# Kernel optimization log

Measured on AMD Instinct MI355X. Metric: run time of the kernel, lower is better.

Reference implementation:

```python
import jax, jax.numpy as jnp
import numpy as np
from jax import lax

NB, D_MODEL, D_INNER, D_STATE, K, L, BATCH, NCLS, DT_RANK = 3, 512, 1024, 8, 4, 2048, 4, 10, 32


def setup_inputs() -> dict:
    key = jax.random.key(0)
    ks = jax.random.split(key, 12)
    s = 0.02
    inp = {
        "x": jax.random.normal(ks[0], (BATCH, L, D_MODEL), jnp.float32),
        "in_proj_w": s * jax.random.normal(ks[1], (NB, D_MODEL, 2 * D_INNER), jnp.float32),
        "conv_w": s * jax.random.normal(ks[2], (NB, D_INNER, K), jnp.float32),
        "conv_b": jnp.zeros((NB, D_INNER), jnp.float32),
        "x_proj_w": s * jax.random.normal(ks[3], (NB, D_INNER, DT_RANK + 2 * D_STATE), jnp.float32),
        "dt_proj_w": s * jax.random.normal(ks[4], (NB, DT_RANK, D_INNER), jnp.float32),
        "dt_proj_b": jnp.full((NB, D_INNER), -4.0, jnp.float32),
        "A_log": jnp.broadcast_to(jnp.log(jnp.arange(1, D_STATE + 1, dtype=jnp.float32)), (NB, D_INNER, D_STATE)).copy(),
        "D": jnp.ones((NB, D_INNER), jnp.float32),
        "out_proj_w": s * jax.random.normal(ks[5], (NB, D_INNER, D_MODEL), jnp.float32),
        "cls_w": s * jax.random.normal(ks[6], (D_MODEL, NCLS), jnp.float32),
        "cls_b": jnp.zeros((NCLS,), jnp.float32),
    }
    return inp


def _mamba_block(x, Wi, cw, cb, Wx, Wdt, bdt, A_log, Dp, Wo):
    # x: [B, L, d_model]
    Bsz, Lx, _ = x.shape
    d_inner = Dp.shape[0]
    d_state = A_log.shape[-1]
    dt_rank = Wdt.shape[0]
    xz = x @ Wi                               # [B, L, 2*d_inner]
    u, z = jnp.split(xz, 2, axis=-1)
    # causal depthwise conv1d over time
    uc = jnp.swapaxes(u, 1, 2)                # [B, d_inner, L]
    k = cw.shape[-1]
    uc = lax.conv_general_dilated(uc, cw[:, None, :], window_strides=(1,),
                                  padding=[(k - 1, 0)], feature_group_count=d_inner,
                                  dimension_numbers=("NCH", "OIH", "NCH"))
    u = jax.nn.silu(jnp.swapaxes(uc, 1, 2) + cb)   # [B, L, d_inner]
    dbl = u @ Wx                                   # [B, L, dt_rank + 2*d_state]
    dt = dbl[..., :dt_rank]
    Bm = dbl[..., dt_rank:dt_rank + d_state]
    Cm = dbl[..., dt_rank + d_state:]
    delta = jax.nn.softplus(dt @ Wdt + bdt)        # [B, L, d_inner]
    A = -jnp.exp(A_log)                            # [d_inner, d_state]

    def step(h, inp):
        d_t, B_t, C_t, u_t = inp                   # [B,d],[B,n],[B,n],[B,d]
        h = jnp.exp(d_t[..., None] * A) * h + (d_t * u_t)[..., None] * B_t[:, None, :]
        return h, jnp.einsum("bdn,bn->bd", h, C_t)

    xs = (jnp.swapaxes(delta, 0, 1), jnp.swapaxes(Bm, 0, 1),
          jnp.swapaxes(Cm, 0, 1), jnp.swapaxes(u, 0, 1))
    h0 = jnp.zeros((Bsz, d_inner, d_state), x.dtype)
    _, ys = lax.scan(step, h0, xs)                 # ys: [L, B, d_inner]
    y = jnp.swapaxes(ys, 0, 1) + u * Dp
    y = y * jax.nn.silu(z)
    return x + y @ Wo                              # residual


def reference(x, in_proj_w, conv_w, conv_b, x_proj_w, dt_proj_w, dt_proj_b, A_log, D, out_proj_w, cls_w, cls_b):
    nb = in_proj_w.shape[0]
    for i in range(nb):
        x = _mamba_block(x, in_proj_w[i], conv_w[i], conv_b[i], x_proj_w[i],
                         dt_proj_w[i], dt_proj_b[i], A_log[i], D[i], out_proj_w[i])
    pooled = jnp.mean(x, axis=1)                   # AdaptiveAvgPool1d(1) over seq
    return pooled @ cls_w + cls_b                  # [B, num_classes]
```

## Files before the change

kernel.cpp:

```cpp
#include <hip/hip_runtime.h>
#include <cstddef>
#include <cstdint>

#define L_SEQ   2048
#define BATCH_N 4
#define DMODEL  512
#define DINNER  1024
#define DSTATE  8
#define KCONV   4
#define DTRANK  32
#define NBLK    3
#define NCLS_N  10
#define MROWS   (BATCH_N * L_SEQ)
#define DBLW    48
#define NSPLIT  8

#define LC2 16
#define NC2 (L_SEQ / LC2)
#define VD  2
#define SCAN_THREADS 512
#define SCAN_WAVES   (SCAN_THREADS / 64)

typedef __attribute__((ext_vector_type(8))) short bf16x8;
typedef __attribute__((ext_vector_type(4))) short bf16x4;
typedef __attribute__((ext_vector_type(2))) short bf16x2;
typedef __attribute__((ext_vector_type(4))) float f32x4;

__device__ __forceinline__ float sigmoid_fast(float x) { return 1.f / (1.f + __expf(-x)); }
__device__ __forceinline__ float silu_fast(float x)    { return x * sigmoid_fast(x); }
__device__ __forceinline__ float softplus_fast(float x){
    return fmaxf(x, 0.f) + __logf(1.f + __expf(-fabsf(x)));
}
__device__ __forceinline__ float exp2_fast(float x) {
#if __has_builtin(__builtin_amdgcn_exp2f)
    return __builtin_amdgcn_exp2f(x);
#else
    return __expf(x * 0.69314718055994531f);
#endif
}
#define LOG2E 1.44269504088896341f

__device__ __forceinline__ unsigned short f2bf(float f) {
    union { float f; uint32_t u; } v; v.f = f;
    const uint32_t u = v.u;
    return (unsigned short)((u + 0x7fffu + ((u >> 16) & 1u)) >> 16);
}
__device__ __forceinline__ float bf2f(unsigned short h) {
    union { uint32_t u; float f; } v; v.u = ((uint32_t)h) << 16;
    return v.f;
}
__device__ __forceinline__ float bf2f_s(short h) { return bf2f((unsigned short)h); }

__device__ __forceinline__ void load_lds16(const void* g, void* l) {
    __builtin_amdgcn_global_load_lds(
        (const __attribute__((address_space(1))) unsigned int*)g,
        (__attribute__((address_space(3))) unsigned int*)l,
        16, 0, 0);
}

template <int K, int NT, int EPI>
__global__ __launch_bounds__(256) void gemm_bf16(
    const unsigned short* __restrict__ A, int lda,
    const unsigned short* __restrict__ Bt, int ldb,
    int ldc,
    unsigned short* __restrict__ Obf,
    float* __restrict__ pool)
{
    constexpr int BCH   = NT / 8;
    constexpr int NTW   = NT / 32;
    constexpr int STAGE = 8192 + NT * 64;
    constexpr int EPIL  = 128 * (NT + 8);
    constexpr int SMEM  = (STAGE > EPIL) ? STAGE : EPIL;
    __shared__ unsigned short sMem[SMEM];
    unsigned short* sA = sMem;
    unsigned short* sB = sMem + 8192;

    const int tid  = threadIdx.x;
    const int lane = tid & 63;
    const int wave = tid >> 6;
    const int m0 = blockIdx.y * 128;
    const int n0 = blockIdx.x * NT;
    const int wm = (wave >> 1) * 64;
    const int wn = (wave & 1) * (NT / 2);
    const int lm = lane & 15;
    const int lq = lane >> 4;

    const int srow = lane >> 3;
    const int scol = ((lane & 7) ^ srow) * 8;

    f32x4 acc[4][NTW];
    #pragma unroll
    for (int i = 0; i < 4; ++i)
        #pragma unroll
        for (int j = 0; j < NTW; ++j) acc[i][j] = (f32x4){0.f, 0.f, 0.f, 0.f};

    for (int k0 = 0; k0 < K; k0 += 64) {
        #pragma unroll
        for (int c = wave; c < 16; c += 4)
            load_lds16(A + (size_t)(m0 + c * 8 + srow) * lda + k0 + scol, &sA[c * 512]);
        #pragma unroll
        for (int c = wave; c < BCH; c += 4)
            load_lds16(Bt + (size_t)(n0 + c * 8 + srow) * ldb + k0 + scol, &sB[c * 512]);
        __syncthreads();
        #pragma unroll
        for (int ks = 0; ks < 2; ++ks) {
            bf16x8 aF[4], bF[NTW];
            #pragma unroll
            for (int mt = 0; mt < 4; ++mt) {
                const int row = wm + mt * 16 + lm;
                aF[mt] = *(const bf16x8*)&sA[row * 64 + (((ks * 4 + lq) ^ (lm & 7)) * 8)];
            }
            #pragma unroll
            for (int nt = 0; nt < NTW; ++nt) {
                const int row = wn + nt * 16 + lm;
                bF[nt] = *(const bf16x8*)&sB[row * 64 + (((ks * 4 + lq) ^ (lm & 7)) * 8)];
            }
            #pragma unroll
            for (int mt = 0; mt < 4; ++mt)
                #pragma unroll
                for (int nt = 0; nt < NTW; ++nt)
                    acc[mt][nt] = __builtin_amdgcn_mfma_f32_16x16x32_bf16(
                        aF[mt], bF[nt], acc[mt][nt], 0, 0, 0);
        }
        __syncthreads();
    }

    unsigned short* sOut = sMem;
    #pragma unroll
    for (int mt = 0; mt < 4; ++mt) {
        #pragma unroll
        for (int nt = 0; nt < NTW; ++nt) {
            #pragma unroll
            for (int r = 0; r < 4; ++r) {
                const int row = wm + mt * 16 + lq * 4 + r;
                const int col = wn + nt * 16 + lm;
                float v = acc[mt][nt][r];
                if (EPI >= 2) {
                    const size_t gi = (size_t)(m0 + row) * ldc + n0 + col;
                    v += bf2f(Obf[gi]);
                }
                sOut[row * (NT + 8) + col] = f2bf(v);
            }
        }
    }
    __syncthreads();
    #pragma unroll
    for (int j = 0; j < NT / 16; ++j) {
        const int idx = j * 256 + tid;
        const int row = idx / (NT / 8);
        const int cpos = (idx % (NT / 8)) * 8;
        *(bf16x8*)&Obf[(size_t)(m0 + row) * ldc + n0 + cpos] =
            *(const bf16x8*)&sOut[row * (NT + 8) + cpos];
    }
    if (EPI == 3) {
        const int b = m0 >> 11;
        const int col = tid & (NT - 1);
        const int q = tid / NT;
        constexpr int RPQ = 128 / (256 / NT);
        float s = 0.f;
        #pragma unroll
        for (int r = q * RPQ; r < (q + 1) * RPQ; ++r)
            s += bf2f(sOut[r * (NT + 8) + col]);
        atomicAdd(&pool[b * DMODEL + n0 + col], s);
    }
}

__global__ __launch_bounds__(256) void gemm_xproj(
    const unsigned short* __restrict__ ub,
    const unsigned short* __restrict__ Wxt,
    float* __restrict__ dblsum)
{
    const int tid = threadIdx.x, lane = tid & 63, wave = tid >> 6;
    const int lm = lane & 15, lq = lane >> 4;
    const int rowA = blockIdx.x * 128 + wave * 32;
    const int split = blockIdx.y;
    const int k0 = split * (DINNER / NSPLIT);

    f32x4 acc[2][3];
    #pragma unroll
    for (int i = 0; i < 2; ++i)
        #pragma unroll
        for (int j = 0; j < 3; ++j) acc[i][j] = (f32x4){0.f, 0.f, 0.f, 0.f};

    #pragma unroll
    for (int kk = 0; kk < DINNER / NSPLIT; kk += 32) {
        const int k = k0 + kk;
        bf16x8 aF[2], bF[3];
        #pragma unroll
        for (int mt = 0; mt < 2; ++mt)
            aF[mt] = *(const bf16x8*)&ub[(size_t)(rowA + mt * 16 + lm) * DINNER + k + lq * 8];
        #pragma unroll
        for (int nt = 0; nt < 3; ++nt)
            bF[nt] = *(const bf16x8*)&Wxt[(size_t)(nt * 16 + lm) * DINNER + k + lq * 8];
        #pragma unroll
        for (int mt = 0; mt < 2; ++mt)
            #pragma unroll
            for (int nt = 0; nt < 3; ++nt)
                acc[mt][nt] = __builtin_amdgcn_mfma_f32_16x16x32_bf16(
                    aF[mt], bF[nt], acc[mt][nt], 0, 0, 0);
    }
    #pragma unroll
    for (int mt = 0; mt < 2; ++mt)
        #pragma unroll
        for (int nt = 0; nt < 3; ++nt)
            #pragma unroll
            for (int r = 0; r < 4; ++r)
                atomicAdd(&dblsum[(size_t)(rowA + mt * 16 + lq * 4 + r) * DBLW
                                  + nt * 16 + lm], acc[mt][nt][r]);
}

__global__ __launch_bounds__(256) void transpose_cast(
    const float* __restrict__ in, unsigned short* __restrict__ out,
    int Kdim, int Ndim, size_t in_stride, size_t out_stride)
{
    __shared__ float s[32][33];
    const float* ip = in + blockIdx.z * in_stride;
    unsigned short* op = out + blockIdx.z * out_stride;
    const int bx = blockIdx.x * 32;
    const int by = blockIdx.y * 32;
    const int t = threadIdx.x;
    const int r = t >> 3;
    const int c4 = (t & 7) * 4;

    const int row = by + r;
    if (bx + c4 + 3 < Ndim) {
        float4 v = *(const float4*)&ip[(size_t)row * Ndim + bx + c4];
        s[r][c4 + 0] = v.x; s[r][c4 + 1] = v.y; s[r][c4 + 2] = v.z; s[r][c4 + 3] = v.w;
    } else {
        for (int i = 0; i < 4; ++i) {
            const int col = bx + c4 + i;
            s[r][c4 + i] = (col < Ndim) ? ip[(size_t)row * Ndim + col] : 0.f;
        }
    }
    __syncthreads();
    if (bx + r < Ndim) {
        unsigned short w0 = f2bf(s[c4 + 0][r]), w1 = f2bf(s[c4 + 1][r]);
        unsigned short w2 = f2bf(s[c4 + 2][r]), w3 = f2bf(s[c4 + 3][r]);
        uint2 pk;
        pk.x = (uint32_t)w0 | ((uint32_t)w1 << 16);
        pk.y = (uint32_t)w2 | ((uint32_t)w3 << 16);
        *(uint2*)&op[(size_t)(bx + r) * Kdim + by + c4] = pk;
    }
}

__global__ void cast_init(const float* __restrict__ in, unsigned short* __restrict__ outb,
                          float* __restrict__ pooled_accum, int n4) {
    const int i = blockIdx.x * 256 + threadIdx.x;
    if (i < BATCH_N * DMODEL / 4)
        ((f32x4*)pooled_accum)[i] = (f32x4){0.f, 0.f, 0.f, 0.f};
    if (i >= n4) return;
    float4 v = ((const float4*)in)[i];
    uint2 pk;
    pk.x = (uint32_t)f2bf(v.x) | ((uint32_t)f2bf(v.y) << 16);
    pk.y = (uint32_t)f2bf(v.z) | ((uint32_t)f2bf(v.w) << 16);
    ((uint2*)outb)[i] = pk;
}

__global__ void conv_w_transpose(const float* __restrict__ cw, float* __restrict__ cwt) {
    const int i = blockIdx.x * 256 + threadIdx.x;
    if (i >= NBLK * DINNER * KCONV) return;
    const int blk = i >> 12;
    const int rem = i & 4095;
    const int d = rem >> 2;
    const int k = rem & 3;
    cwt[blk * 4096 + k * DINNER + d] = cw[blk * 4096 + d * KCONV + k];
}

__global__ __launch_bounds__(256) void conv_silu_kernel(
    const unsigned short* __restrict__ xz,
    const float* __restrict__ cwt,
    const float* __restrict__ cb,
    unsigned short* __restrict__ ub,
    float* __restrict__ dblsum)
{
    const int idx = blockIdx.x * 256 + threadIdx.x;
    if (idx < MROWS * DBLW / 4)
        ((f32x4*)dblsum)[idx] = (f32x4){0.f, 0.f, 0.f, 0.f};

    const int dv = idx & 127;
    const int m  = idx >> 7;
    const int t  = m & (L_SEQ - 1);
    const int d0 = dv * 8;

    float acc[8];
    {
        float4 c0 = *(const float4*)&cb[d0];
        float4 c1 = *(const float4*)&cb[d0 + 4];
        acc[0] = c0.x; acc[1] = c0.y; acc[2] = c0.z; acc[3] = c0.w;
        acc[4] = c1.x; acc[5] = c1.y; acc[6] = c1.z; acc[7] = c1.w;
    }
    #pragma unroll
    for (int k = 0; k < KCONV; ++k) {
        const int tt = t + k - (KCONV - 1);
        if (tt >= 0) {
            bf16x8 xv = *(const bf16x8*)&xz[(size_t)(m - t + tt) * (2 * DINNER) + d0];
            float4 w0 = *(const float4*)&cwt[k * DINNER + d0];
            float4 w1 = *(const float4*)&cwt[k * DINNER + d0 + 4];
            acc[0] = fmaf(bf2f_s(xv[0]), w0.x, acc[0]);
            acc[1] = fmaf(bf2f_s(xv[1]), w0.y, acc[1]);
            acc[2] = fmaf(bf2f_s(xv[2]), w0.z, acc[2]);
            acc[3] = fmaf(bf2f_s(xv[3]), w0.w, acc[3]);
            acc[4] = fmaf(bf2f_s(xv[4]), w1.x, acc[4]);
            acc[5] = fmaf(bf2f_s(xv[5]), w1.y, acc[5]);
            acc[6] = fmaf(bf2f_s(xv[6]), w1.z, acc[6]);
            acc[7] = fmaf(bf2f_s(xv[7]), w1.w, acc[7]);
        }
    }
    bf16x8 o;
    #pragma unroll
    for (int j = 0; j < 8; ++j) o[j] = (short)f2bf(silu_fast(acc[j]));
    *(bf16x8*)&ub[(size_t)m * DINNER + d0] = o;
}

__device__ __forceinline__ void dt_recompute_lds(
    unsigned short* sDelta,
    const float* __restrict__ dblsum,
    const unsigned short* __restrict__ Wdtt,
    const float* __restrict__ bdt,
    size_t m0, int lane, int wave)
{
    const int lm = lane & 15, lq = lane >> 4;
    bf16x8 aF;
    {
        const float* p = &dblsum[(m0 + lm) * DBLW + lq * 8];
        float4 x0 = *(const float4*)p;
        float4 x1 = *(const float4*)(p + 4);
        aF[0] = (short)f2bf(x0.x); aF[1] = (short)f2bf(x0.y);
        aF[2] = (short)f2bf(x0.z); aF[3] = (short)f2bf(x0.w);
        aF[4] = (short)f2bf(x1.x); aF[5] = (short)f2bf(x1.y);
        aF[6] = (short)f2bf(x1.z); aF[7] = (short)f2bf(x1.w);
    }
    constexpr int NPW = DINNER / (16 * SCAN_WAVES);
    #pragma unroll
    for (int nt = 0; nt < NPW; ++nt) {
        const int col16 = wave * (DINNER / SCAN_WAVES) + nt * 16;
        bf16x8 bF = *(const bf16x8*)&Wdtt[(size_t)(col16 + lm) * DTRANK + lq * 8];
        f32x4 acc = (f32x4){0.f, 0.f, 0.f, 0.f};
        acc = __builtin_amdgcn_mfma_f32_16x16x32_bf16(aF, bF, acc, 0, 0, 0);
        const float bias = bdt[col16 + lm];
        #pragma unroll
        for (int r = 0; r < 4; ++r)
            sDelta[(lq * 4 + r) * DINNER + col16 + lm] =
                f2bf(softplus_fast(acc[r] + bias));
    }
}

__global__ __launch_bounds__(SCAN_THREADS) void scan_chunk_kernel(
    const unsigned short* __restrict__ ub,
    const float* __restrict__ dblsum,
    const unsigned short* __restrict__ Wdtt,
    const float* __restrict__ bdt,
    const float* __restrict__ A_log,
    float* __restrict__ PSbuf)
{
    const int c = blockIdx.x;
    const int b = blockIdx.y;
    const int tid = threadIdx.x;
    const int lane = tid & 63;
    const int wave = tid >> 6;
    const int d0 = tid * VD;

    __shared__ unsigned short sDelta[LC2 * DINNER];
    __shared__ float sB[LC2][DSTATE];

    const size_t m0 = (size_t)b * L_SEQ + c * LC2;

    dt_recompute_lds(sDelta, dblsum, Wdtt, bdt, m0, lane, wave);
    if (tid < LC2 * DSTATE) {
        const int r = tid >> 3, n = tid & 7;
        sB[r][n] = dblsum[(m0 + r) * DBLW + DTRANK + n];
    }
    __syncthreads();

    float a[DSTATE * VD], P[DSTATE * VD], S[DSTATE * VD];
    #pragma unroll
    for (int n = 0; n < DSTATE; ++n)
        #pragma unroll
        for (int v = 0; v < VD; ++v) {
            a[n * VD + v] = -__expf(A_log[(d0 + v) * DSTATE + n]) * LOG2E;
            P[n * VD + v] = 1.f;
            S[n * VD + v] = 0.f;
        }

    for (int r = 0; r < LC2; ++r) {
        const size_t m = m0 + r;
        bf16x2 dv = *(const bf16x2*)&sDelta[r * DINNER + d0];
        bf16x2 uv = *(const bf16x2*)&ub[m * DINNER + d0];
        float dt[VD], du[VD];
        #pragma unroll
        for (int v = 0; v < VD; ++v) {
            dt[v] = bf2f_s(dv[v]);
            du[v] = dt[v] * bf2f_s(uv[v]);
        }
        #pragma unroll
        for (int n = 0; n < DSTATE; ++n) {
            const float bn = sB[r][n];
            #pragma unroll
            for (int v = 0; v < VD; ++v) {
                const float e = exp2_fast(dt[v] * a[n * VD + v]);
                S[n * VD + v] = fmaf(e, S[n * VD + v], du[v] * bn);
                P[n * VD + v] *= e;
            }
        }
    }

    const size_t nb = (size_t)(b * NC2 + c) * DSTATE;
    #pragma unroll
    for (int n = 0; n < DSTATE; ++n) {
        float* dst = &PSbuf[(nb + n) * (DINNER * 2) + (size_t)d0 * 2];
        *(f32x4*)dst =
            (f32x4){P[n * VD + 0], S[n * VD + 0], P[n * VD + 1], S[n * VD + 1]};
    }
}

__global__ __launch_bounds__(64) void scan_combine_kernel(
    const float* __restrict__ PSbuf,
    float* __restrict__ Hbuf)
{
    const int d = blockIdx.x * 64 + threadIdx.x;
    const int n = blockIdx.y;
    const int b = blockIdx.z;

    float h = 0.f;
    #pragma unroll 8
    for (int c = 0; c < NC2; ++c) {
        const size_t row = (size_t)(b * NC2 + c) * DSTATE + n;
        const float2 ps = *(const float2*)&PSbuf[row * (DINNER * 2) + (size_t)d * 2];
        Hbuf[row * DINNER + d] = h;
        h = fmaf(ps.x, h, ps.y);
    }
}

__global__ __launch_bounds__(SCAN_THREADS) void scan_out_kernel(
    const unsigned short* __restrict__ ub,
    const float* __restrict__ dblsum,
    const unsigned short* __restrict__ Wdtt,
    const float* __restrict__ bdt,
    const unsigned short* __restrict__ xz,
    const float* __restrict__ A_log,
    const float* __restrict__ Dp,
    const float* __restrict__ Hin,
    unsigned short* __restrict__ ybuf)
{
    const int c = blockIdx.x;
    const int b = blockIdx.y;
    const int tid = threadIdx.x;
    const int lane = tid & 63;
    const int wave = tid >> 6;
    const int d0 = tid * VD;

    __shared__ unsigned short sDelta[LC2 * DINNER];
    __shared__ float sB[LC2][DSTATE];
    __shared__ float sC[LC2][DSTATE];

    const size_t m0 = (size_t)b * L_SEQ + c * LC2;

    dt_recompute_lds(sDelta, dblsum, Wdtt, bdt, m0, lane, wave);
    if (tid < LC2 * 2 * DSTATE) {
        const int r = tid >> 4, j = tid & 15;
        const float v = dblsum[(m0 + r) * DBLW + DTRANK + j];
        if (j < DSTATE) sB[r][j] = v;
        else            sC[r][j - DSTATE] = v;
    }
    __syncthreads();

    float a[DSTATE * VD], h[DSTATE * VD];
    const size_t base = ((size_t)(b * NC2 + c) * DSTATE) * DINNER + d0;
    #pragma unroll
    for (int n = 0; n < DSTATE; ++n) {
        float2 hv = *(const float2*)&Hin[base + (size_t)n * DINNER];
        h[n * VD + 0] = hv.x; h[n * VD + 1] = hv.y;
        #pragma unroll
        for (int v = 0; v < VD; ++v)
            a[n * VD + v] = -__expf(A_log[(d0 + v) * DSTATE + n]) * LOG2E;
    }
    float Dd[VD];
    {
        float2 dv2 = *(const float2*)&Dp[d0];
        Dd[0] = dv2.x; Dd[1] = dv2.y;
    }

    for (int r = 0; r < LC2; ++r) {
        const size_t m = m0 + r;
        bf16x2 dv = *(const bf16x2*)&sDelta[r * DINNER + d0];
        bf16x2 uv = *(const bf16x2*)&ub[m * DINNER + d0];
        bf16x2 zv = *(const bf16x2*)&xz[m * (2 * DINNER) + DINNER + d0];
        float dt[VD], ut[VD], du[VD], acc[VD];
        #pragma unroll
        for (int v = 0; v < VD; ++v) {
            dt[v] = bf2f_s(dv[v]);
            ut[v] = bf2f_s(uv[v]);
            du[v] = dt[v] * ut[v];
            acc[v] = 0.f;
        }
        #pragma unroll
        for (int n = 0; n < DSTATE; ++n) {
            const float bn = sB[r][n];
            const float cn = sC[r][n];
            #pragma unroll
            for (int v = 0; v < VD; ++v) {
                const float e = exp2_fast(dt[v] * a[n * VD + v]);
                h[n * VD + v] = fmaf(e, h[n * VD + v], du[v] * bn);
                acc[v] = fmaf(h[n * VD + v], cn, acc[v]);
            }
        }
        bf16x2 o;
        #pragma unroll
        for (int v = 0; v < VD; ++v)
            o[v] = (short)f2bf(fmaf(ut[v], Dd[v], acc[v]) * silu_fast(bf2f_s(zv[v])));
        *(bf16x2*)&ybuf[m * DINNER + d0] = o;
    }
}

__global__ __launch_bounds__(512) void pool_cls_kernel(
    const float* __restrict__ pooled_accum,
    const float* __restrict__ w,
    const float* __restrict__ bias,
    float* __restrict__ out)
{
    __shared__ float sp[DMODEL];
    const int b = blockIdx.x;
    const int dm = threadIdx.x;
    sp[dm] = pooled_accum[b * DMODEL + dm] * (1.f / (float)L_SEQ);
    __syncthreads();
    if (dm < NCLS_N) {
        float acc = bias[dm];
        for (int k = 0; k < DMODEL; ++k)
            acc = fmaf(sp[k], w[k * NCLS_N + dm], acc);
        out[b * NCLS_N + dm] = acc;
    }
}

extern "C" void kernel_launch(void* const* d_in, const int* in_sizes, int n_in,
                              void* d_out, int out_size, void* d_ws, size_t ws_size,
                              hipStream_t stream) {
    const float* x_in      = (const float*)d_in[0];
    const float* in_proj_w = (const float*)d_in[1];
    const float* conv_w    = (const float*)d_in[2];
    const float* conv_b    = (const float*)d_in[3];
    const float* x_proj_w  = (const float*)d_in[4];
    const float* dt_proj_w = (const float*)d_in[5];
    const float* dt_proj_b = (const float*)d_in[6];
    const float* A_log     = (const float*)d_in[7];
    const float* Dp        = (const float*)d_in[8];
    const float* out_proj_w= (const float*)d_in[9];
    const float* cls_w     = (const float*)d_in[10];
    const float* cls_b     = (const float*)d_in[11];
    float* out = (float*)d_out;

    char* w = (char*)d_ws;
    auto alloc = [&](size_t bytes) { char* p = w; w += (bytes + 255) & ~(size_t)255; return p; };
    unsigned short* xz_bf  = (unsigned short*)alloc((size_t)MROWS * 2 * DINNER * 2);
    unsigned short* ub     = (unsigned short*)alloc((size_t)MROWS * DINNER * 2);
    float*          dblsum = (float*)         alloc((size_t)MROWS * DBLW * 4);
    float*          PSbuf  = (float*)         alloc((size_t)BATCH_N * NC2 * DSTATE * DINNER * 2 * 4);
    float*          Hbuf   = (float*)         alloc((size_t)BATCH_N * NC2 * DSTATE * DINNER * 4);
    unsigned short* xb     = (unsigned short*)alloc((size_t)MROWS * DMODEL * 2);
    unsigned short* ybuf   = (unsigned short*)alloc((size_t)MROWS * DINNER * 2);
    unsigned short* Wit    = (unsigned short*)alloc((size_t)NBLK * 2048 * 512 * 2);
    unsigned short* Wot    = (unsigned short*)alloc((size_t)NBLK * 512 * 1024 * 2);
    unsigned short* Wxt    = (unsigned short*)alloc((size_t)NBLK * DBLW * 1024 * 2);
    unsigned short* Wdtt   = (unsigned short*)alloc((size_t)NBLK * 1024 * DTRANK * 2);
    float*          cwt    = (float*)         alloc((size_t)NBLK * KCONV * DINNER * 4);
    float*          pooled = (float*)         alloc((size_t)BATCH_N * DMODEL * 4);

    cast_init<<<(MROWS * DMODEL / 4) / 256, 256, 0, stream>>>(
        x_in, xb, pooled, MROWS * DMODEL / 4);
    transpose_cast<<<dim3(2048 / 32, 512 / 32, NBLK), 256, 0, stream>>>(
        in_proj_w, Wit, 512, 2048, (size_t)512 * 2048, (size_t)2048 * 512);
    transpose_cast<<<dim3(512 / 32, 1024 / 32, NBLK), 256, 0, stream>>>(
        out_proj_w, Wot, 1024, 512, (size_t)1024 * 512, (size_t)512 * 1024);
    transpose_cast<<<dim3(2, 1024 / 32, NBLK), 256, 0, stream>>>(
        x_proj_w, Wxt, 1024, DBLW, (size_t)1024 * DBLW, (size_t)DBLW * 1024);
    transpose_cast<<<dim3(1024 / 32, 1, NBLK), 256, 0, stream>>>(
        dt_proj_w, Wdtt, DTRANK, 1024, (size_t)DTRANK * 1024, (size_t)1024 * DTRANK);
    conv_w_transpose<<<(NBLK * DINNER * KCONV + 255) / 256, 256, 0, stream>>>(conv_w, cwt);

    for (int blk = 0; blk < NBLK; ++blk) {
        const unsigned short* Wit_b  = Wit  + (size_t)blk * 2048 * 512;
        const unsigned short* Wot_b  = Wot  + (size_t)blk * 512 * 1024;
        const unsigned short* Wxt_b  = Wxt  + (size_t)blk * DBLW * 1024;
        const unsigned short* Wdtt_b = Wdtt + (size_t)blk * 1024 * DTRANK;
        const float* cwt_b = cwt + (size_t)blk * KCONV * DINNER;
        const float* cb  = conv_b    + (size_t)blk * DINNER;
        const float* bdt = dt_proj_b + (size_t)blk * DINNER;
        const float* Al  = A_log     + (size_t)blk * DINNER * DSTATE;
        const float* Dv  = Dp        + (size_t)blk * DINNER;

        gemm_bf16<512, 128, 0><<<dim3(2048 / 128, MROWS / 128), 256, 0, stream>>>(
            xb, DMODEL, Wit_b, DMODEL, 2 * DINNER, xz_bf, nullptr);
        conv_silu_kernel<<<(MROWS * 128) / 256, 256, 0, stream>>>(
            xz_bf, cwt_b, cb, ub, dblsum);
        gemm_xproj<<<dim3(MROWS / 128, NSPLIT), 256, 0, stream>>>(ub, Wxt_b, dblsum);
        {
            dim3 gridA(NC2, BATCH_N);
            scan_chunk_kernel<<<gridA, SCAN_THREADS, 0, stream>>>(
                ub, dblsum, Wdtt_b, bdt, Al, PSbuf);
            scan_combine_kernel<<<dim3(DINNER / 64, DSTATE, BATCH_N), 64, 0, stream>>>(
                PSbuf, Hbuf);
            scan_out_kernel<<<gridA, SCAN_THREADS, 0, stream>>>(
                ub, dblsum, Wdtt_b, bdt, xz_bf, Al, Dv, Hbuf, ybuf);
        }
        if (blk < NBLK - 1)
            gemm_bf16<1024, 64, 2><<<dim3(DMODEL / 64, MROWS / 128), 256, 0, stream>>>(
                ybuf, DINNER, Wot_b, DINNER, DMODEL, xb, nullptr);
        else
            gemm_bf16<1024, 64, 3><<<dim3(DMODEL / 64, MROWS / 128), 256, 0, stream>>>(
                ybuf, DINNER, Wot_b, DINNER, DMODEL, xb, pooled);
    }

    pool_cls_kernel<<<BATCH_N, DMODEL, 0, stream>>>(pooled, cls_w, cls_b, out);
}
```

Measured before the change: 533.4 us.

## Replace split-K atomics with partial buffers and parallelize chunk-prefix combine

The x_proj split-K GEMM now writes each split's partial sums to its own buffer instead of atomically adding into a zeroed buffer, and the scan kernels sum the eight partials when they load. The conv kernel no longer zeroes that buffer. The chunk decay product is computed as exp2 of a times the summed dt instead of a running per-step product. The cross-chunk combine kernel splits the 128 chunks into 8 groups per block, building group prefixes in LDS so the serial chain is shorter. The cost is more reads of the partial buffers in the scan kernels and extra workspace.

```diff
diff --git a/kernel.cpp b/kernel.cpp
--- a/kernel.cpp
+++ b/kernel.cpp
@@ -21,6 +21,9 @@
 #define SCAN_THREADS 512
 #define SCAN_WAVES   (SCAN_THREADS / 64)
 
+#define CGRP 8
+#define CPG  (NC2 / CGRP)
+
 typedef __attribute__((ext_vector_type(8))) short bf16x8;
 typedef __attribute__((ext_vector_type(4))) short bf16x4;
 typedef __attribute__((ext_vector_type(2))) short bf16x2;
@@ -168,7 +171,7 @@
 __global__ __launch_bounds__(256) void gemm_xproj(
     const unsigned short* __restrict__ ub,
     const unsigned short* __restrict__ Wxt,
-    float* __restrict__ dblsum)
+    float* __restrict__ Xp)
 {
     const int tid = threadIdx.x, lane = tid & 63, wave = tid >> 6;
     const int lm = lane & 15, lq = lane >> 4;
@@ -199,14 +202,15 @@
                 acc[mt][nt] = __builtin_amdgcn_mfma_f32_16x16x32_bf16(
                     aF[mt], bF[nt], acc[mt][nt], 0, 0, 0);
     }
+    float* dst = Xp + (size_t)split * MROWS * DBLW;
     #pragma unroll
     for (int mt = 0; mt < 2; ++mt)
         #pragma unroll
         for (int nt = 0; nt < 3; ++nt)
             #pragma unroll
             for (int r = 0; r < 4; ++r)
-                atomicAdd(&dblsum[(size_t)(rowA + mt * 16 + lq * 4 + r) * DBLW
-                                  + nt * 16 + lm], acc[mt][nt][r]);
+                dst[(size_t)(rowA + mt * 16 + lq * 4 + r) * DBLW
+                    + nt * 16 + lm] = acc[mt][nt][r];
 }
 
 __global__ __launch_bounds__(256) void transpose_cast(
@@ -270,13 +274,9 @@
     const unsigned short* __restrict__ xz,
     const float* __restrict__ cwt,
     const float* __restrict__ cb,
-    unsigned short* __restrict__ ub,
-    float* __restrict__ dblsum)
+    unsigned short* __restrict__ ub)
 {
     const int idx = blockIdx.x * 256 + threadIdx.x;
-    if (idx < MROWS * DBLW / 4)
-        ((f32x4*)dblsum)[idx] = (f32x4){0.f, 0.f, 0.f, 0.f};
-
     const int dv = idx & 127;
     const int m  = idx >> 7;
     const int t  = m & (L_SEQ - 1);
@@ -314,22 +314,25 @@
 
 __device__ __forceinline__ void dt_recompute_lds(
     unsigned short* sDelta,
-    const float* __restrict__ dblsum,
+    const float* __restrict__ Xp,
     const unsigned short* __restrict__ Wdtt,
     const float* __restrict__ bdt,
     size_t m0, int lane, int wave)
 {
     const int lm = lane & 15, lq = lane >> 4;
-    bf16x8 aF;
-    {
-        const float* p = &dblsum[(m0 + lm) * DBLW + lq * 8];
+    float x[8] = {0.f, 0.f, 0.f, 0.f, 0.f, 0.f, 0.f, 0.f};
+    #pragma unroll
+    for (int sp = 0; sp < NSPLIT; ++sp) {
+        const float* p = &Xp[((size_t)sp * MROWS + m0 + lm) * DBLW + lq * 8];
         float4 x0 = *(const float4*)p;
         float4 x1 = *(const float4*)(p + 4);
-        aF[0] = (short)f2bf(x0.x); aF[1] = (short)f2bf(x0.y);
-        aF[2] = (short)f2bf(x0.z); aF[3] = (short)f2bf(x0.w);
-        aF[4] = (short)f2bf(x1.x); aF[5] = (short)f2bf(x1.y);
-        aF[6] = (short)f2bf(x1.z); aF[7] = (short)f2bf(x1.w);
-    }
+        x[0] += x0.x; x[1] += x0.y; x[2] += x0.z; x[3] += x0.w;
+        x[4] += x1.x; x[5] += x1.y; x[6] += x1.z; x[7] += x1.w;
+    }
+    bf16x8 aF;
+    #pragma unroll
+    for (int j = 0; j < 8; ++j) aF[j] = (short)f2bf(x[j]);
+
     constexpr int NPW = DINNER / (16 * SCAN_WAVES);
     #pragma unroll
     for (int nt = 0; nt < NPW; ++nt) {
@@ -347,7 +350,7 @@
 
 __global__ __launch_bounds__(SCAN_THREADS) void scan_chunk_kernel(
     const unsigned short* __restrict__ ub,
-    const float* __restrict__ dblsum,
+    const float* __restrict__ Xp,
     const unsigned short* __restrict__ Wdtt,
     const float* __restrict__ bdt,
     const float* __restrict__ A_log,
@@ -365,20 +368,26 @@
 
     const size_t m0 = (size_t)b * L_SEQ + c * LC2;
 
-    dt_recompute_lds(sDelta, dblsum, Wdtt, bdt, m0, lane, wave);
+    dt_recompute_lds(sDelta, Xp, Wdtt, bdt, m0, lane, wave);
     if (tid < LC2 * DSTATE) {
         const int r = tid >> 3, n = tid & 7;
-        sB[r][n] = dblsum[(m0 + r) * DBLW + DTRANK + n];
+        float s = 0.f;
+        #pragma unroll
+        for (int sp = 0; sp < NSPLIT; ++sp)
+            s += Xp[((size_t)sp * MROWS + m0 + r) * DBLW + DTRANK + n];
+        sB[r][n] = s;
     }
     __syncthreads();
 
-    float a[DSTATE * VD], P[DSTATE * VD], S[DSTATE * VD];
+    float a[DSTATE * VD], S[DSTATE * VD];
+    float dtsum[VD];
+    #pragma unroll
+    for (int v = 0; v < VD; ++v) dtsum[v] = 0.f;
     #pragma unroll
     for (int n = 0; n < DSTATE; ++n)
         #pragma unroll
         for (int v = 0; v < VD; ++v) {
             a[n * VD + v] = -__expf(A_log[(d0 + v) * DSTATE + n]) * LOG2E;
-            P[n * VD + v] = 1.f;
             S[n * VD + v] = 0.f;
         }
 
@@ -391,6 +400,7 @@
         for (int v = 0; v < VD; ++v) {
             dt[v] = bf2f_s(dv[v]);
             du[v] = dt[v] * bf2f_s(uv[v]);
+            dtsum[v] += dt[v];
         }
         #pragma unroll
         for (int n = 0; n < DSTATE; ++n) {
@@ -399,7 +409,6 @@
             for (int v = 0; v < VD; ++v) {
                 const float e = exp2_fast(dt[v] * a[n * VD + v]);
                 S[n * VD + v] = fmaf(e, S[n * VD + v], du[v] * bn);
-                P[n * VD + v] *= e;
             }
         }
     }
@@ -407,24 +416,46 @@
     const size_t nb = (size_t)(b * NC2 + c) * DSTATE;
     #pragma unroll
     for (int n = 0; n < DSTATE; ++n) {
+        const float P0 = exp2_fast(a[n * VD + 0] * dtsum[0]);
+        const float P1 = exp2_fast(a[n * VD + 1] * dtsum[1]);
         float* dst = &PSbuf[(nb + n) * (DINNER * 2) + (size_t)d0 * 2];
-        *(f32x4*)dst =
-            (f32x4){P[n * VD + 0], S[n * VD + 0], P[n * VD + 1], S[n * VD + 1]};
-    }
-}
-
-__global__ __launch_bounds__(64) void scan_combine_kernel(
+        *(f32x4*)dst = (f32x4){P0, S[n * VD + 0], P1, S[n * VD + 1]};
+    }
+}
+
+__global__ __launch_bounds__(512) void scan_combine_kernel(
     const float* __restrict__ PSbuf,
     float* __restrict__ Hbuf)
 {
-    const int d = blockIdx.x * 64 + threadIdx.x;
-    const int n = blockIdx.y;
-    const int b = blockIdx.z;
+    const int dl = threadIdx.x & 63;
+    const int g  = threadIdx.x >> 6;
+    const int d  = blockIdx.x * 64 + dl;
+    const int n  = blockIdx.y;
+    const int b  = blockIdx.z;
+
+    __shared__ float sP[CGRP][64];
+    __shared__ float sS[CGRP][64];
+
+    const int c0 = g * CPG;
+    float Pseg = 1.f, Sseg = 0.f;
+    #pragma unroll 4
+    for (int cc = 0; cc < CPG; ++cc) {
+        const size_t row = (size_t)(b * NC2 + c0 + cc) * DSTATE + n;
+        const float2 ps = *(const float2*)&PSbuf[row * (DINNER * 2) + (size_t)d * 2];
+        Pseg *= ps.x;
+        Sseg = fmaf(ps.x, Sseg, ps.y);
+    }
+    sP[g][dl] = Pseg;
+    sS[g][dl] = Sseg;
+    __syncthreads();
 
     float h = 0.f;
-    #pragma unroll 8
-    for (int c = 0; c < NC2; ++c) {
-        const size_t row = (size_t)(b * NC2 + c) * DSTATE + n;
+    for (int gg = 0; gg < g; ++gg)
+        h = fmaf(sP[gg][dl], h, sS[gg][dl]);
+
+    #pragma unroll 4
+    for (int cc = 0; cc < CPG; ++cc) {
+        const size_t row = (size_t)(b * NC2 + c0 + cc) * DSTATE + n;
         const float2 ps = *(const float2*)&PSbuf[row * (DINNER * 2) + (size_t)d * 2];
         Hbuf[row * DINNER + d] = h;
         h = fmaf(ps.x, h, ps.y);
@@ -433,7 +464,7 @@
 
 __global__ __launch_bounds__(SCAN_THREADS) void scan_out_kernel(
     const unsigned short* __restrict__ ub,
-    const float* __restrict__ dblsum,
+    const float* __restrict__ Xp,
     const unsigned short* __restrict__ Wdtt,
     const float* __restrict__ bdt,
     const unsigned short* __restrict__ xz,
@@ -455,12 +486,15 @@
 
     const size_t m0 = (size_t)b * L_SEQ + c * LC2;
 
-    dt_recompute_lds(sDelta, dblsum, Wdtt, bdt, m0, lane, wave);
+    dt_recompute_lds(sDelta, Xp, Wdtt, bdt, m0, lane, wave);
     if (tid < LC2 * 2 * DSTATE) {
         const int r = tid >> 4, j = tid & 15;
-        const float v = dblsum[(m0 + r) * DBLW + DTRANK + j];
-        if (j < DSTATE) sB[r][j] = v;
-        else            sC[r][j - DSTATE] = v;
+        float s = 0.f;
+        #pragma unroll
+        for (int sp = 0; sp < NSPLIT; ++sp)
+            s += Xp[((size_t)sp * MROWS + m0 + r) * DBLW + DTRANK + j];
+        if (j < DSTATE) sB[r][j] = s;
+        else            sC[r][j - DSTATE] = s;
     }
     __syncthreads();
 
@@ -552,7 +586,7 @@
     auto alloc = [&](size_t bytes) { char* p = w; w += (bytes + 255) & ~(size_t)255; return p; };
     unsigned short* xz_bf  = (unsigned short*)alloc((size_t)MROWS * 2 * DINNER * 2);
     unsigned short* ub     = (unsigned short*)alloc((size_t)MROWS * DINNER * 2);
-    float*          dblsum = (float*)         alloc((size_t)MROWS * DBLW * 4);
+    float*          Xp     = (float*)         alloc((size_t)NSPLIT * MROWS * DBLW * 4);
     float*          PSbuf  = (float*)         alloc((size_t)BATCH_N * NC2 * DSTATE * DINNER * 2 * 4);
     float*          Hbuf   = (float*)         alloc((size_t)BATCH_N * NC2 * DSTATE * DINNER * 4);
     unsigned short* xb     = (unsigned short*)alloc((size_t)MROWS * DMODEL * 2);
@@ -590,16 +624,16 @@
         gemm_bf16<512, 128, 0><<<dim3(2048 / 128, MROWS / 128), 256, 0, stream>>>(
             xb, DMODEL, Wit_b, DMODEL, 2 * DINNER, xz_bf, nullptr);
         conv_silu_kernel<<<(MROWS * 128) / 256, 256, 0, stream>>>(
-            xz_bf, cwt_b, cb, ub, dblsum);
-        gemm_xproj<<<dim3(MROWS / 128, NSPLIT), 256, 0, stream>>>(ub, Wxt_b, dblsum);
+            xz_bf, cwt_b, cb, ub);
+        gemm_xproj<<<dim3(MROWS / 128, NSPLIT), 256, 0, stream>>>(ub, Wxt_b, Xp);
         {
             dim3 gridA(NC2, BATCH_N);
             scan_chunk_kernel<<<gridA, SCAN_THREADS, 0, stream>>>(
-                ub, dblsum, Wdtt_b, bdt, Al, PSbuf);
-            scan_combine_kernel<<<dim3(DINNER / 64, DSTATE, BATCH_N), 64, 0, stream>>>(
+                ub, Xp, Wdtt_b, bdt, Al, PSbuf);
+            scan_combine_kernel<<<dim3(DINNER / 64, DSTATE, BATCH_N), 512, 0, stream>>>(
                 PSbuf, Hbuf);
             scan_out_kernel<<<gridA, SCAN_THREADS, 0, stream>>>(
-                ub, dblsum, Wdtt_b, bdt, xz_bf, Al, Dv, Hbuf, ybuf);
+                ub, Xp, Wdtt_b, bdt, xz_bf, Al, Dv, Hbuf, ybuf);
         }
         if (blk < NBLK - 1)
             gemm_bf16<1024, 64, 2><<<dim3(DMODEL / 64, MROWS / 128), 256, 0, stream>>>(
```

After: 551.1 us. 3.3% more time.
